# Optimization experiments

Hardware: AMD Instinct MI355X
Metric: run time of the kernel (lower is better)

## Reference

```python
import jax, jax.numpy as jnp
import numpy as np
import math

N = 65536   # number of tree nodes
K = 4       # branching factor of the complete K-ary tree
D = 300     # input_size
H = 256     # hidden_size

def _levels(n, k):
    # complete k-ary tree: level l spans [start, start + k**l)
    levels, start, size = [], 0, 1
    while start < n:
        end = min(start + size, n)
        levels.append((start, end))
        start, size = end, size * k
    return levels

LEVELS = _levels(N, K)

def setup_inputs() -> dict:
    key = jax.random.key(0)
    ks = jax.random.split(key, 16)
    def U(k, shape, s):
        return jax.random.uniform(k, shape, jnp.float32, -s, s)
    s1 = 1.0 / math.sqrt(D + H)
    sfi = 1.0 / math.sqrt(D)
    sfh = 1.0 / math.sqrt(H)
    return {
        "inputs": jax.random.normal(ks[0], (N, D), jnp.float32),
        "ix_w": U(ks[1], (H, D), s1), "ix_b": U(ks[2], (H,), s1),
        "ih_w": U(ks[3], (H, H), s1), "ih_b": U(ks[4], (H,), s1),
        "ux_w": U(ks[5], (H, D), s1), "ux_b": U(ks[6], (H,), s1),
        "uh_w": U(ks[7], (H, H), s1), "uh_b": U(ks[8], (H,), s1),
        "fi_w": U(ks[9], (H, D), sfi), "fi_b": U(ks[10], (H,), sfi),
        "fh_w": U(ks[11], (H, H), sfh), "fh_b": U(ks[12], (H,), sfh),
    }

def reference(inputs, ix_w, ix_b, ih_w, ih_b, ux_w, ux_b, uh_w, uh_b,
              fi_w, fi_b, fh_w, fh_b):
    # Precompute all input projections once (batched over every node).
    ix = inputs @ ix_w.T + ix_b   # [N, H]
    ux = inputs @ ux_w.T + ux_b   # [N, H]
    fi = inputs @ fi_w.T + fi_b   # [N, H]
    h = jnp.zeros((N, H), inputs.dtype)
    c = jnp.zeros((N, H), inputs.dtype)
    # Bottom-up over tree levels (children before parents); level bounds static.
    for (s, e) in reversed(LEVELS):
        node = jnp.arange(s, e)                                   # [L]
        cidx = node[:, None] * K + 1 + jnp.arange(K)[None, :]     # [L, K]
        valid = cidx < N
        cidx = jnp.where(valid, cidx, 0)
        m = valid[..., None].astype(inputs.dtype)                 # [L, K, 1]
        hc = h[cidx] * m                                          # [L, K, H]
        cc = c[cidx] * m
        h_sum = hc.sum(axis=1)                                    # [L, H]
        # per-child forget gate: sigmoid(W_fi x + b_fi + W_fh h_k + b_fh)
        f = jax.nn.sigmoid(fi[s:e][:, None, :]
                           + jnp.einsum('lkh,gh->lkg', hc, fh_w) + fh_b)
        fc = (f * cc).sum(axis=1)                                 # masked via cc
        i = jax.nn.sigmoid(ix[s:e] + h_sum @ ih_w.T + ih_b)
        u = jnp.tanh(ux[s:e] + h_sum @ uh_w.T + uh_b)
        c_new = i * u + fc
        h_new = jnp.tanh(c_new)          # no output gate in this module
        h = h.at[s:e].set(h_new)
        c = c.at[s:e].set(c_new)
    # root node state (matches (next_h, [next_h, next_c]) at the root)
    return h[0], c[0]
```

## Files before the change

kernel.cpp:

```cpp
#include <hip/hip_runtime.h>
#include <hip/hip_bf16.h>


#define NTOT 65536
#define DD   300
#define KP   320
#define HH   256
#define LEAF_START 16384
#define LOG2E 1.4426950408889634f

typedef unsigned short u16;
typedef unsigned int   u32;
typedef __attribute__((ext_vector_type(8))) short bf16x8;
typedef __attribute__((ext_vector_type(4))) float f32x4;

union BF8 { bf16x8 v; u16 u[8]; };

#define OFF_HB    0ull
#define OFF_CB    33554944ull
#define OFF_PRE   67109888ull
#define OFF_WXB   92275712ull
#define OFF_WHB   92767232ull
#define OFF_XB    93160448ull
#define OFF_PIU   135103488ull
#define OFF_PF    146375680ull
#define OFF_BI    168788992ull
#define OFF_BU    168790016ull
#define OFF_BF    168791040ull

__device__ __forceinline__ float frcp(float x) { return __builtin_amdgcn_rcpf(x); }
__device__ __forceinline__ float fex2(float x) { return __builtin_amdgcn_exp2f(x); }
__device__ __forceinline__ float sigm(float x)  { return frcp(1.f + fex2(-LOG2E * x)); }
__device__ __forceinline__ float ftanh(float x) { return 1.f - 2.f * frcp(1.f + fex2(2.f * LOG2E * x)); }

__device__ __forceinline__ u16 f2bf(float f) {
    __hip_bfloat16 b = __float2bfloat16(f);
    u16 u; __builtin_memcpy(&u, &b, 2); return u;
}
__device__ __forceinline__ float bf2f(u16 b) {
    union { u32 u; float f; } v; v.u = ((u32)b) << 16;
    return v.f;
}
__device__ __forceinline__ int lidx(int r, int g) { return (r << 3) | (g ^ (r & 7)); }

__device__ __forceinline__ void gll16(const void* g, void* l) {
    __builtin_amdgcn_global_load_lds(
        (const __attribute__((address_space(1))) unsigned int*)g,
        (__attribute__((address_space(3))) unsigned int*)l, 16, 0, 0);
}

__global__ __launch_bounds__(256) void conv_x(const float* __restrict__ X,
                                              u32* __restrict__ Xb2) {
    const size_t total = (size_t)NTOT * (KP / 2);
    for (size_t id = (size_t)blockIdx.x * 256 + threadIdx.x; id < total;
         id += (size_t)gridDim.x * 256) {
        const int node = (int)(id / (KP / 2));
        const int k    = ((int)(id % (KP / 2))) * 2;
        const float f0 = (k < DD)     ? X[(size_t)node * DD + k]     : 0.f;
        const float f1 = (k + 1 < DD) ? X[(size_t)node * DD + k + 1] : 0.f;
        Xb2[id] = (u32)f2bf(f0) | ((u32)f2bf(f1) << 16);
    }
}

__global__ __launch_bounds__(256) void conv_wx(const float* __restrict__ ixw,
                                               const float* __restrict__ uxw,
                                               const float* __restrict__ fiw,
                                               u32* __restrict__ W2) {
    const int total = 768 * (KP / 2);
    for (int id = blockIdx.x * 256 + threadIdx.x; id < total;
         id += gridDim.x * 256) {
        const int row = id / (KP / 2);
        const int k   = (id % (KP / 2)) * 2;
        const float* src = (row < 256) ? (ixw + (size_t)row * DD)
                         : (row < 512) ? (uxw + (size_t)(row - 256) * DD)
                                       : (fiw + (size_t)(row - 512) * DD);
        const float f0 = (k < DD)     ? src[k]     : 0.f;
        const float f1 = (k + 1 < DD) ? src[k + 1] : 0.f;
        W2[id] = (u32)f2bf(f0) | ((u32)f2bf(f1) << 16);
    }
}

__global__ __launch_bounds__(256) void conv_wh(const float* __restrict__ ihw,
                                               const float* __restrict__ uhw,
                                               const float* __restrict__ fhw,
                                               const float* __restrict__ ixb,
                                               const float* __restrict__ ihb,
                                               const float* __restrict__ uxb,
                                               const float* __restrict__ uhb,
                                               const float* __restrict__ fib,
                                               const float* __restrict__ fhb,
                                               u32* __restrict__ W2,
                                               u16* __restrict__ hb,
                                               u16* __restrict__ cb,
                                               float* __restrict__ bI,
                                               float* __restrict__ bU,
                                               float* __restrict__ bF) {
    if (blockIdx.x == 0) {
        const int t = threadIdx.x;
        hb[(size_t)NTOT * HH + t] = 0;
        cb[(size_t)NTOT * HH + t] = 0;
        bI[t] = ixb[t] + ihb[t];
        bU[t] = uxb[t] + uhb[t];
        bF[t] = fib[t] + fhb[t];
    }
    const int total = 768 * (HH / 2);
    for (int id = blockIdx.x * 256 + threadIdx.x; id < total;
         id += gridDim.x * 256) {
        const int row = id / (HH / 2);
        const int k   = (id % (HH / 2)) * 2;
        const float* src = (row < 256) ? (ihw + (size_t)row * HH)
                         : (row < 512) ? (uhw + (size_t)(row - 256) * HH)
                                       : (fhw + (size_t)(row - 512) * HH);
        W2[id] = (u32)f2bf(src[k]) | ((u32)f2bf(src[k + 1]) << 16);
    }
}

__global__ __launch_bounds__(256) void leaf_gemm(
    const u16* __restrict__ Xb, const u16* __restrict__ Wxb,
    const float* __restrict__ bI, const float* __restrict__ bU,
    u16* __restrict__ hb, u16* __restrict__ cb)
{
    __shared__ bf16x8 Ash[1024];
    __shared__ bf16x8 Bsh[1024];

    const int tid  = threadIdx.x;
    const int lane = tid & 63;
    const int w    = tid >> 6;
    const int wr   = w >> 1, wc = w & 1;
    const int m16  = lane & 15, q = lane >> 4;

    const int row0   = LEAF_START + blockIdx.x * 128;
    const int chbase = blockIdx.y * 64;

    const bf16x8* __restrict__ Xv = (const bf16x8*)Xb;
    const bf16x8* __restrict__ Wv = (const bf16x8*)Wxb;

    f32x4 accI[4][2], accU[4][2];
    #pragma unroll
    for (int mf = 0; mf < 4; ++mf)
        #pragma unroll
        for (int nf = 0; nf < 2; ++nf) { accI[mf][nf] = (f32x4)0.f; accU[mf][nf] = (f32x4)0.f; }

    for (int kt = 0; kt < 5; ++kt) {
        __syncthreads();
        #pragma unroll
        for (int i = 0; i < 4; ++i) {
            const int s = w * 256 + i * 64 + lane;
            const int r = s >> 3, gs = s & 7;
            const int g = gs ^ (r & 7);
            gll16(Xv + (size_t)(row0 + r) * 40 + kt * 8 + g, &Ash[s]);
        }
        #pragma unroll
        for (int i = 0; i < 4; ++i) {
            const int s = w * 256 + i * 64 + lane;
            const int br = s >> 3, gs = s & 7;
            const int g = gs ^ (br & 7);
            const int srow = ((br >> 6) << 8) + chbase + (br & 63);
            gll16(Wv + (size_t)srow * 40 + kt * 8 + g, &Bsh[s]);
        }
        __syncthreads();

        #pragma unroll
        for (int ks = 0; ks < 2; ++ks) {
            const int kg = ks * 4 + q;
            bf16x8 a[4], bIv[2], bUv[2];
            #pragma unroll
            for (int mf = 0; mf < 4; ++mf)
                a[mf] = Ash[lidx(wr * 64 + mf * 16 + m16, kg)];
            #pragma unroll
            for (int nf = 0; nf < 2; ++nf) {
                bIv[nf] = Bsh[lidx(wc * 32 + nf * 16 + m16, kg)];
                bUv[nf] = Bsh[lidx(64 + wc * 32 + nf * 16 + m16, kg)];
            }
            #pragma unroll
            for (int mf = 0; mf < 4; ++mf)
                #pragma unroll
                for (int nf = 0; nf < 2; ++nf) {
                    accI[mf][nf] = __builtin_amdgcn_mfma_f32_16x16x32_bf16(
                        a[mf], bIv[nf], accI[mf][nf], 0, 0, 0);
                    accU[mf][nf] = __builtin_amdgcn_mfma_f32_16x16x32_bf16(
                        a[mf], bUv[nf], accU[mf][nf], 0, 0, 0);
                }
        }
    }

    #pragma unroll
    for (int nf = 0; nf < 2; ++nf) {
        const int ch = chbase + wc * 32 + nf * 16 + m16;
        const float bi = bI[ch];
        const float bu = bU[ch];
        #pragma unroll
        for (int mf = 0; mf < 4; ++mf) {
            #pragma unroll
            for (int r4 = 0; r4 < 4; ++r4) {
                const float cn = sigm(accI[mf][nf][r4] + bi) * ftanh(accU[mf][nf][r4] + bu);
                const int node = row0 + wr * 64 + mf * 16 + q * 4 + r4;
                const size_t off = (size_t)node * HH + ch;
                cb[off] = f2bf(cn);
                hb[off] = f2bf(ftanh(cn));
            }
        }
    }
}

__global__ __launch_bounds__(256) void proj_gemm(const u16* __restrict__ Xb,
                                                 const u16* __restrict__ Wxb,
                                                 u16* __restrict__ pre)
{
    __shared__ bf16x8 Ash[1024];
    __shared__ bf16x8 Bsh[1024];

    const int tid  = threadIdx.x;
    const int lane = tid & 63;
    const int w    = tid >> 6;
    const int wr   = w >> 1, wc = w & 1;
    const int m16  = lane & 15, q = lane >> 4;

    const int row0 = blockIdx.x * 128;
    const int n0   = blockIdx.y * 128;

    const bf16x8* __restrict__ Xv = (const bf16x8*)Xb;
    const bf16x8* __restrict__ Wv = (const bf16x8*)Wxb;

    f32x4 acc[4][4];
    #pragma unroll
    for (int mf = 0; mf < 4; ++mf)
        #pragma unroll
        for (int nf = 0; nf < 4; ++nf) acc[mf][nf] = (f32x4)0.f;

    for (int kt = 0; kt < 5; ++kt) {
        __syncthreads();
        #pragma unroll
        for (int i = 0; i < 4; ++i) {
            const int s = w * 256 + i * 64 + lane;
            const int r = s >> 3, gs = s & 7;
            const int g = gs ^ (r & 7);
            gll16(Xv + (size_t)(row0 + r) * 40 + kt * 8 + g, &Ash[s]);
        }
        #pragma unroll
        for (int i = 0; i < 4; ++i) {
            const int s = w * 256 + i * 64 + lane;
            const int br = s >> 3, gs = s & 7;
            const int g = gs ^ (br & 7);
            gll16(Wv + (size_t)(n0 + br) * 40 + kt * 8 + g, &Bsh[s]);
        }
        __syncthreads();

        #pragma unroll
        for (int ks = 0; ks < 2; ++ks) {
            const int kg = ks * 4 + q;
            bf16x8 a[4], b[4];
            #pragma unroll
            for (int mf = 0; mf < 4; ++mf)
                a[mf] = Ash[lidx(wr * 64 + mf * 16 + m16, kg)];
            #pragma unroll
            for (int nf = 0; nf < 4; ++nf)
                b[nf] = Bsh[lidx(wc * 64 + nf * 16 + m16, kg)];
            #pragma unroll
            for (int mf = 0; mf < 4; ++mf)
                #pragma unroll
                for (int nf = 0; nf < 4; ++nf)
                    acc[mf][nf] = __builtin_amdgcn_mfma_f32_16x16x32_bf16(
                        a[mf], b[nf], acc[mf][nf], 0, 0, 0);
        }
    }

    #pragma unroll
    for (int mf = 0; mf < 4; ++mf)
        #pragma unroll
        for (int nf = 0; nf < 4; ++nf) {
            const int col = n0 + wc * 64 + nf * 16 + m16;
            #pragma unroll
            for (int r4 = 0; r4 < 4; ++r4) {
                const int node = row0 + wr * 64 + mf * 16 + q * 4 + r4;
                pre[(size_t)node * 768 + col] = f2bf(acc[mf][nf][r4]);
            }
        }
}

__global__ __launch_bounds__(256) void rec_gemm(const u16* __restrict__ hb,
                                                const u16* __restrict__ Whb,
                                                u16* __restrict__ projIU,
                                                u16* __restrict__ projF,
                                                int crow0, int L)
{
    __shared__ bf16x8 Ash[1024];
    __shared__ bf16x8 Bsh[1024];

    const int nIUrb = (L + 127) >> 7;
    const int bid   = blockIdx.x;

    bool isIU; int rb, cb_;
    if (bid < nIUrb * 4) { isIU = true;  rb = bid >> 2; cb_ = bid & 3; }
    else { isIU = false; const int b2 = bid - nIUrb * 4; rb = b2 >> 1; cb_ = b2 & 1; }

    const int row0  = rb * 128;
    const int Brow0 = isIU ? cb_ * 128 : 512 + cb_ * 128;
    const int ocol0 = cb_ * 128;
    u16* __restrict__ out = isIU ? projIU : projF;
    const int ostride = isIU ? 512 : 256;

    const int tid  = threadIdx.x;
    const int lane = tid & 63;
    const int w    = tid >> 6;
    const int wr   = w >> 1, wc = w & 1;
    const int m16  = lane & 15, q = lane >> 4;

    const bf16x8* __restrict__ Hv = (const bf16x8*)hb;
    const bf16x8* __restrict__ Wv = (const bf16x8*)Whb;

    f32x4 acc[4][4];
    #pragma unroll
    for (int mf = 0; mf < 4; ++mf)
        #pragma unroll
        for (int nf = 0; nf < 4; ++nf) acc[mf][nf] = (f32x4)0.f;

    for (int kt = 0; kt < 4; ++kt) {
        __syncthreads();
        if (isIU) {
            #pragma unroll
            for (int i = 0; i < 4; ++i) {
                const int G = tid + i * 256;
                const int r = G >> 3, g = G & 7;
                bf16x8 val;
                if (row0 + r < L) {
                    const size_t cg0 = (size_t)(crow0 + 4 * (row0 + r)) * 32 + kt * 8 + g;
                    BF8 x0, x1, x2, x3, o;
                    x0.v = Hv[cg0]; x1.v = Hv[cg0 + 32];
                    x2.v = Hv[cg0 + 64]; x3.v = Hv[cg0 + 96];
                    #pragma unroll
                    for (int j = 0; j < 8; ++j)
                        o.u[j] = f2bf(bf2f(x0.u[j]) + bf2f(x1.u[j])
                                    + bf2f(x2.u[j]) + bf2f(x3.u[j]));
                    val = o.v;
                } else {
                    BF8 z;
                    #pragma unroll
                    for (int j = 0; j < 8; ++j) z.u[j] = 0;
                    val = z.v;
                }
                Ash[lidx(r, g)] = val;
            }
        } else {
            #pragma unroll
            for (int i = 0; i < 4; ++i) {
                const int s = w * 256 + i * 64 + lane;
                const int r = s >> 3, gs = s & 7;
                const int g = gs ^ (r & 7);
                int srow = crow0 + row0 + r;
                if (srow > NTOT) srow = NTOT;
                gll16(Hv + (size_t)srow * 32 + kt * 8 + g, &Ash[s]);
            }
        }
        #pragma unroll
        for (int i = 0; i < 4; ++i) {
            const int s = w * 256 + i * 64 + lane;
            const int br = s >> 3, gs = s & 7;
            const int g = gs ^ (br & 7);
            gll16(Wv + (size_t)(Brow0 + br) * 32 + kt * 8 + g, &Bsh[s]);
        }
        __syncthreads();

        #pragma unroll
        for (int ks = 0; ks < 2; ++ks) {
            const int kg = ks * 4 + q;
            bf16x8 a[4], b[4];
            #pragma unroll
            for (int mf = 0; mf < 4; ++mf)
                a[mf] = Ash[lidx(wr * 64 + mf * 16 + m16, kg)];
            #pragma unroll
            for (int nf = 0; nf < 4; ++nf)
                b[nf] = Bsh[lidx(wc * 64 + nf * 16 + m16, kg)];
            #pragma unroll
            for (int mf = 0; mf < 4; ++mf)
                #pragma unroll
                for (int nf = 0; nf < 4; ++nf)
                    acc[mf][nf] = __builtin_amdgcn_mfma_f32_16x16x32_bf16(
                        a[mf], b[nf], acc[mf][nf], 0, 0, 0);
        }
    }

    #pragma unroll
    for (int mf = 0; mf < 4; ++mf)
        #pragma unroll
        for (int nf = 0; nf < 4; ++nf) {
            const int col = ocol0 + wc * 64 + nf * 16 + m16;
            #pragma unroll
            for (int r4 = 0; r4 < 4; ++r4) {
                const int orow = row0 + wr * 64 + mf * 16 + q * 4 + r4;
                out[(size_t)orow * ostride + col] = f2bf(acc[mf][nf][r4]);
            }
        }
}

__global__ __launch_bounds__(256) void gate_kernel(
    const u32* __restrict__ pre2, const u32* __restrict__ pIU2,
    const u32* __restrict__ pF2,
    const float* __restrict__ bI, const float* __restrict__ bU,
    const float* __restrict__ bF,
    u32* __restrict__ hb2, u32* __restrict__ cb2, float* __restrict__ out,
    int s, int crow0, int L)
{
    const int t    = threadIdx.x;
    const int half = t >> 7;
    const int j2   = t & 127;
    const int nloc = blockIdx.x * 2 + half;
    if (nloc >= L) return;
    const int n = s + nloc;

    const u32 pi = pre2[(size_t)n * 384 + j2];
    const u32 pu = pre2[(size_t)n * 384 + 128 + j2];
    const u32 pf = pre2[(size_t)n * 384 + 256 + j2];
    const u32 ri = pIU2[(size_t)nloc * 256 + j2];
    const u32 ru = pIU2[(size_t)nloc * 256 + 128 + j2];
    const float2 vbi = ((const float2*)bI)[j2];
    const float2 vbu = ((const float2*)bU)[j2];
    const float2 vbf = ((const float2*)bF)[j2];

    const float aI0 = bf2f((u16)pi) + bf2f((u16)ri) + vbi.x;
    const float aI1 = bf2f((u16)(pi >> 16)) + bf2f((u16)(ri >> 16)) + vbi.y;
    const float aU0 = bf2f((u16)pu) + bf2f((u16)ru) + vbu.x;
    const float aU1 = bf2f((u16)(pu >> 16)) + bf2f((u16)(ru >> 16)) + vbu.y;
    const float fp0 = bf2f((u16)pf) + vbf.x;
    const float fp1 = bf2f((u16)(pf >> 16)) + vbf.y;

    float fc0 = 0.f, fc1 = 0.f;
    #pragma unroll
    for (int k = 0; k < 4; ++k) {
        const u32 rf = pF2[(size_t)(4 * nloc + k) * 128 + j2];
        const u32 cc = cb2[(size_t)(crow0 + 4 * nloc + k) * 128 + j2];
        fc0 = fmaf(sigm(fp0 + bf2f((u16)rf)), bf2f((u16)cc), fc0);
        fc1 = fmaf(sigm(fp1 + bf2f((u16)(rf >> 16))), bf2f((u16)(cc >> 16)), fc1);
    }
    const float cn0 = fmaf(sigm(aI0), ftanh(aU0), fc0);
    const float cn1 = fmaf(sigm(aI1), ftanh(aU1), fc1);
    const float hn0 = ftanh(cn0);
    const float hn1 = ftanh(cn1);
    hb2[(size_t)n * 128 + j2] = (u32)f2bf(hn0) | ((u32)f2bf(hn1) << 16);
    cb2[(size_t)n * 128 + j2] = (u32)f2bf(cn0) | ((u32)f2bf(cn1) << 16);
    if (n == 0) {
        ((float2*)out)[j2] = make_float2(hn0, hn1);
        ((float2*)(out + 256))[j2] = make_float2(cn0, cn1);
    }
}

extern "C" void kernel_launch(void* const* d_in, const int* in_sizes, int n_in,
                              void* d_out, int out_size, void* d_ws, size_t ws_size,
                              hipStream_t stream) {
    const float* X   = (const float*)d_in[0];
    const float* ixw = (const float*)d_in[1];
    const float* ixb = (const float*)d_in[2];
    const float* ihw = (const float*)d_in[3];
    const float* ihb = (const float*)d_in[4];
    const float* uxw = (const float*)d_in[5];
    const float* uxb = (const float*)d_in[6];
    const float* uhw = (const float*)d_in[7];
    const float* uhb = (const float*)d_in[8];
    const float* fiw = (const float*)d_in[9];
    const float* fib = (const float*)d_in[10];
    const float* fhw = (const float*)d_in[11];
    const float* fhb = (const float*)d_in[12];
    float* out = (float*)d_out;

    char* ws = (char*)d_ws;
    u16* hb  = (u16*)(ws + OFF_HB);
    u16* cb  = (u16*)(ws + OFF_CB);
    u16* pre = (u16*)(ws + OFF_PRE);
    u16* Wxb = (u16*)(ws + OFF_WXB);
    u16* Whb = (u16*)(ws + OFF_WHB);
    u16* Xb  = (u16*)(ws + OFF_XB);
    u16* pIU = (u16*)(ws + OFF_PIU);
    u16* pF  = (u16*)(ws + OFF_PF);
    float* bI = (float*)(ws + OFF_BI);
    float* bU = (float*)(ws + OFF_BU);
    float* bF = (float*)(ws + OFF_BF);

    conv_wx<<<480, 256, 0, stream>>>(ixw, uxw, fiw, (u32*)Wxb);
    conv_wh<<<384, 256, 0, stream>>>(ihw, uhw, fhw, ixb, ihb, uxb, uhb, fib, fhb,
                                     (u32*)Whb, hb, cb, bI, bU, bF);
    conv_x <<<2048, 256, 0, stream>>>(X, (u32*)Xb);

    leaf_gemm<<<dim3(384, 4), 256, 0, stream>>>(Xb, Wxb, bI, bU, hb, cb);
    proj_gemm<<<dim3(128, 6), 256, 0, stream>>>(Xb, Wxb, pre);

    const int starts[8] = {5461, 1365, 341, 85, 21, 5, 1, 0};
    const int ends[8]   = {16384, 5461, 1365, 341, 85, 21, 5, 1};
    for (int l = 0; l < 8; ++l) {
        const int s = starts[l], e = ends[l];
        const int L = e - s;
        const int crow0 = 4 * s + 1;
        const int nIUrb = (L + 127) >> 7;
        const int nFrb  = (4 * L + 127) >> 7;
        rec_gemm<<<nIUrb * 4 + nFrb * 2, 256, 0, stream>>>(hb, Whb, pIU, pF, crow0, L);
        gate_kernel<<<(L + 1) >> 1, 256, 0, stream>>>(
            (const u32*)pre, (const u32*)pIU, (const u32*)pF, bI, bU, bF,
            (u32*)hb, (u32*)cb, out, s, crow0, L);
    }
}
```

Measured before the change: 213.2 us.

## Fuse conversion kernels, double-buffer GEMM LDS, precompute child h-sums in gate kernel

Merges the three bf16 conversion kernels into a single launch. Leaf, projection and recurrent GEMMs now double-buffer their LDS tiles so the next k-tile's global-to-LDS loads overlap the current MFMAs. Child hidden-state sums are computed ahead of time: a new kernel handles the leaf level, and the gate kernel emits parent sums, so rec_gemm's IU path loads them directly with async LDS loads instead of summing four children per tile. The cost is extra LDS per block, a new workspace buffer, and an extra bf16 rounding of the summed hidden state.

```diff
diff --git a/kernel.cpp b/kernel.cpp
--- a/kernel.cpp
+++ b/kernel.cpp
@@ -13,8 +13,6 @@
 typedef unsigned int   u32;
 typedef __attribute__((ext_vector_type(8))) short bf16x8;
 typedef __attribute__((ext_vector_type(4))) float f32x4;
-
-union BF8 { bf16x8 v; u16 u[8]; };
 
 #define OFF_HB    0ull
 #define OFF_CB    33554944ull
@@ -24,9 +22,10 @@
 #define OFF_XB    93160448ull
 #define OFF_PIU   135103488ull
 #define OFF_PF    146375680ull
-#define OFF_BI    168788992ull
-#define OFF_BU    168790016ull
-#define OFF_BF    168791040ull
+#define OFF_HSB   168788992ull
+#define OFF_BI    177243136ull
+#define OFF_BU    177244160ull
+#define OFF_BF    177245184ull
 
 __device__ __forceinline__ float frcp(float x) { return __builtin_amdgcn_rcpf(x); }
 __device__ __forceinline__ float fex2(float x) { return __builtin_amdgcn_exp2f(x); }
@@ -49,69 +48,61 @@
         (__attribute__((address_space(3))) unsigned int*)l, 16, 0, 0);
 }
 
-__global__ __launch_bounds__(256) void conv_x(const float* __restrict__ X,
-                                              u32* __restrict__ Xb2) {
-    const size_t total = (size_t)NTOT * (KP / 2);
-    for (size_t id = (size_t)blockIdx.x * 256 + threadIdx.x; id < total;
-         id += (size_t)gridDim.x * 256) {
-        const int node = (int)(id / (KP / 2));
-        const int k    = ((int)(id % (KP / 2))) * 2;
-        const float f0 = (k < DD)     ? X[(size_t)node * DD + k]     : 0.f;
-        const float f1 = (k + 1 < DD) ? X[(size_t)node * DD + k + 1] : 0.f;
-        Xb2[id] = (u32)f2bf(f0) | ((u32)f2bf(f1) << 16);
-    }
-}
-
-__global__ __launch_bounds__(256) void conv_wx(const float* __restrict__ ixw,
-                                               const float* __restrict__ uxw,
-                                               const float* __restrict__ fiw,
-                                               u32* __restrict__ W2) {
-    const int total = 768 * (KP / 2);
-    for (int id = blockIdx.x * 256 + threadIdx.x; id < total;
-         id += gridDim.x * 256) {
-        const int row = id / (KP / 2);
-        const int k   = (id % (KP / 2)) * 2;
-        const float* src = (row < 256) ? (ixw + (size_t)row * DD)
-                         : (row < 512) ? (uxw + (size_t)(row - 256) * DD)
-                                       : (fiw + (size_t)(row - 512) * DD);
-        const float f0 = (k < DD)     ? src[k]     : 0.f;
-        const float f1 = (k + 1 < DD) ? src[k + 1] : 0.f;
-        W2[id] = (u32)f2bf(f0) | ((u32)f2bf(f1) << 16);
-    }
-}
-
-__global__ __launch_bounds__(256) void conv_wh(const float* __restrict__ ihw,
-                                               const float* __restrict__ uhw,
-                                               const float* __restrict__ fhw,
-                                               const float* __restrict__ ixb,
-                                               const float* __restrict__ ihb,
-                                               const float* __restrict__ uxb,
-                                               const float* __restrict__ uhb,
-                                               const float* __restrict__ fib,
-                                               const float* __restrict__ fhb,
-                                               u32* __restrict__ W2,
-                                               u16* __restrict__ hb,
-                                               u16* __restrict__ cb,
-                                               float* __restrict__ bI,
-                                               float* __restrict__ bU,
-                                               float* __restrict__ bF) {
-    if (blockIdx.x == 0) {
-        const int t = threadIdx.x;
-        hb[(size_t)NTOT * HH + t] = 0;
-        cb[(size_t)NTOT * HH + t] = 0;
-        bI[t] = ixb[t] + ihb[t];
-        bU[t] = uxb[t] + uhb[t];
-        bF[t] = fib[t] + fhb[t];
-    }
-    const int total = 768 * (HH / 2);
-    for (int id = blockIdx.x * 256 + threadIdx.x; id < total;
-         id += gridDim.x * 256) {
-        const int row = id / (HH / 2);
-        const int k   = (id % (HH / 2)) * 2;
-        const float* src = (row < 256) ? (ihw + (size_t)row * HH)
-                         : (row < 512) ? (uhw + (size_t)(row - 256) * HH)
-                                       : (fhw + (size_t)(row - 512) * HH);
-        W2[id] = (u32)f2bf(src[k]) | ((u32)f2bf(src[k + 1]) << 16);
+__global__ __launch_bounds__(256) void conv_all(
+    const float* __restrict__ X,
+    const float* __restrict__ ixw, const float* __restrict__ uxw,
+    const float* __restrict__ fiw,
+    const float* __restrict__ ihw, const float* __restrict__ uhw,
+    const float* __restrict__ fhw,
+    const float* __restrict__ ixb, const float* __restrict__ ihb,
+    const float* __restrict__ uxb, const float* __restrict__ uhb,
+    const float* __restrict__ fib, const float* __restrict__ fhb,
+    u32* __restrict__ Xb2, u32* __restrict__ Wxb2, u32* __restrict__ Whb2,
+    u16* __restrict__ hb, u16* __restrict__ cb,
+    float* __restrict__ bI, float* __restrict__ bU, float* __restrict__ bF)
+{
+    const int b = blockIdx.x;
+    const int t = threadIdx.x;
+    if (b < 2048) {
+        const size_t total = (size_t)NTOT * 160;
+        for (size_t id = (size_t)b * 256 + t; id < total; id += (size_t)2048 * 256) {
+            const int node = (int)(id / 160);
+            const int k    = ((int)(id % 160)) * 2;
+            const float f0 = (k < DD)     ? X[(size_t)node * DD + k]     : 0.f;
+            const float f1 = (k + 1 < DD) ? X[(size_t)node * DD + k + 1] : 0.f;
+            Xb2[id] = (u32)f2bf(f0) | ((u32)f2bf(f1) << 16);
+        }
+    } else if (b < 2528) {
+        const int b2 = b - 2048;
+        const int total = 768 * 160;
+        for (int id = b2 * 256 + t; id < total; id += 480 * 256) {
+            const int row = id / 160;
+            const int k   = (id % 160) * 2;
+            const float* src = (row < 256) ? (ixw + (size_t)row * DD)
+                             : (row < 512) ? (uxw + (size_t)(row - 256) * DD)
+                                           : (fiw + (size_t)(row - 512) * DD);
+            const float f0 = (k < DD)     ? src[k]     : 0.f;
+            const float f1 = (k + 1 < DD) ? src[k + 1] : 0.f;
+            Wxb2[id] = (u32)f2bf(f0) | ((u32)f2bf(f1) << 16);
+        }
+    } else {
+        const int b3 = b - 2528;
+        if (b3 == 0) {
+            hb[(size_t)NTOT * HH + t] = 0;
+            cb[(size_t)NTOT * HH + t] = 0;
+            bI[t] = ixb[t] + ihb[t];
+            bU[t] = uxb[t] + uhb[t];
+            bF[t] = fib[t] + fhb[t];
+        }
+        const int total = 768 * 128;
+        for (int id = b3 * 256 + t; id < total; id += 384 * 256) {
+            const int row = id / 128;
+            const int k   = (id % 128) * 2;
+            const float* src = (row < 256) ? (ihw + (size_t)row * HH)
+                             : (row < 512) ? (uhw + (size_t)(row - 256) * HH)
+                                           : (fhw + (size_t)(row - 512) * HH);
+            Whb2[id] = (u32)f2bf(src[k]) | ((u32)f2bf(src[k + 1]) << 16);
+        }
     }
 }
 
@@ -120,8 +111,8 @@
     const float* __restrict__ bI, const float* __restrict__ bU,
     u16* __restrict__ hb, u16* __restrict__ cb)
 {
-    __shared__ bf16x8 Ash[1024];
-    __shared__ bf16x8 Bsh[1024];
+    __shared__ bf16x8 Ash[2048];
+    __shared__ bf16x8 Bsh[2048];
 
     const int tid  = threadIdx.x;
     const int lane = tid & 63;
@@ -135,42 +126,48 @@
     const bf16x8* __restrict__ Xv = (const bf16x8*)Xb;
     const bf16x8* __restrict__ Wv = (const bf16x8*)Wxb;
 
-    f32x4 accI[4][2], accU[4][2];
-    #pragma unroll
-    for (int mf = 0; mf < 4; ++mf)
-        #pragma unroll
-        for (int nf = 0; nf < 2; ++nf) { accI[mf][nf] = (f32x4)0.f; accU[mf][nf] = (f32x4)0.f; }
-
-    for (int kt = 0; kt < 5; ++kt) {
-        __syncthreads();
+    auto stage = [&](int kt, int buf) {
+        const int base = buf << 10;
         #pragma unroll
         for (int i = 0; i < 4; ++i) {
-            const int s = w * 256 + i * 64 + lane;
-            const int r = s >> 3, gs = s & 7;
+            const int sI = w * 256 + i * 64 + lane;
+            const int r = sI >> 3, gs = sI & 7;
             const int g = gs ^ (r & 7);
-            gll16(Xv + (size_t)(row0 + r) * 40 + kt * 8 + g, &Ash[s]);
+            gll16(Xv + (size_t)(row0 + r) * 40 + kt * 8 + g, &Ash[base + sI]);
         }
         #pragma unroll
         for (int i = 0; i < 4; ++i) {
-            const int s = w * 256 + i * 64 + lane;
-            const int br = s >> 3, gs = s & 7;
+            const int sI = w * 256 + i * 64 + lane;
+            const int br = sI >> 3, gs = sI & 7;
             const int g = gs ^ (br & 7);
             const int srow = ((br >> 6) << 8) + chbase + (br & 63);
-            gll16(Wv + (size_t)srow * 40 + kt * 8 + g, &Bsh[s]);
-        }
-        __syncthreads();
-
+            gll16(Wv + (size_t)srow * 40 + kt * 8 + g, &Bsh[base + sI]);
+        }
+    };
+
+    f32x4 accI[4][2], accU[4][2];
+    #pragma unroll
+    for (int mf = 0; mf < 4; ++mf)
+        #pragma unroll
+        for (int nf = 0; nf < 2; ++nf) { accI[mf][nf] = (f32x4)0.f; accU[mf][nf] = (f32x4)0.f; }
+
+    stage(0, 0);
+    __syncthreads();
+    for (int kt = 0; kt < 5; ++kt) {
+        const int cur = kt & 1;
+        if (kt < 4) stage(kt + 1, cur ^ 1);
+        const int base = cur << 10;
         #pragma unroll
         for (int ks = 0; ks < 2; ++ks) {
             const int kg = ks * 4 + q;
             bf16x8 a[4], bIv[2], bUv[2];
             #pragma unroll
             for (int mf = 0; mf < 4; ++mf)
-                a[mf] = Ash[lidx(wr * 64 + mf * 16 + m16, kg)];
+                a[mf] = Ash[base + lidx(wr * 64 + mf * 16 + m16, kg)];
             #pragma unroll
             for (int nf = 0; nf < 2; ++nf) {
-                bIv[nf] = Bsh[lidx(wc * 32 + nf * 16 + m16, kg)];
-                bUv[nf] = Bsh[lidx(64 + wc * 32 + nf * 16 + m16, kg)];
+                bIv[nf] = Bsh[base + lidx(wc * 32 + nf * 16 + m16, kg)];
+                bUv[nf] = Bsh[base + lidx(64 + wc * 32 + nf * 16 + m16, kg)];
             }
             #pragma unroll
             for (int mf = 0; mf < 4; ++mf)
@@ -182,6 +179,7 @@
                         a[mf], bUv[nf], accU[mf][nf], 0, 0, 0);
                 }
         }
+        __syncthreads();
     }
 
     #pragma unroll
@@ -207,8 +205,8 @@
                                                  const u16* __restrict__ Wxb,
                                                  u16* __restrict__ pre)
 {
-    __shared__ bf16x8 Ash[1024];
-    __shared__ bf16x8 Bsh[1024];
+    __shared__ bf16x8 Ash[2048];
+    __shared__ bf16x8 Bsh[2048];
 
     const int tid  = threadIdx.x;
     const int lane = tid & 63;
@@ -222,40 +220,46 @@
     const bf16x8* __restrict__ Xv = (const bf16x8*)Xb;
     const bf16x8* __restrict__ Wv = (const bf16x8*)Wxb;
 
+    auto stage = [&](int kt, int buf) {
+        const int base = buf << 10;
+        #pragma unroll
+        for (int i = 0; i < 4; ++i) {
+            const int sI = w * 256 + i * 64 + lane;
+            const int r = sI >> 3, gs = sI & 7;
+            const int g = gs ^ (r & 7);
+            gll16(Xv + (size_t)(row0 + r) * 40 + kt * 8 + g, &Ash[base + sI]);
+        }
+        #pragma unroll
+        for (int i = 0; i < 4; ++i) {
+            const int sI = w * 256 + i * 64 + lane;
+            const int br = sI >> 3, gs = sI & 7;
+            const int g = gs ^ (br & 7);
+            gll16(Wv + (size_t)(n0 + br) * 40 + kt * 8 + g, &Bsh[base + sI]);
+        }
+    };
+
     f32x4 acc[4][4];
     #pragma unroll
     for (int mf = 0; mf < 4; ++mf)
         #pragma unroll
         for (int nf = 0; nf < 4; ++nf) acc[mf][nf] = (f32x4)0.f;
 
+    stage(0, 0);
+    __syncthreads();
     for (int kt = 0; kt < 5; ++kt) {
-        __syncthreads();
-        #pragma unroll
-        for (int i = 0; i < 4; ++i) {
-            const int s = w * 256 + i * 64 + lane;
-            const int r = s >> 3, gs = s & 7;
-            const int g = gs ^ (r & 7);
-            gll16(Xv + (size_t)(row0 + r) * 40 + kt * 8 + g, &Ash[s]);
-        }
-        #pragma unroll
-        for (int i = 0; i < 4; ++i) {
-            const int s = w * 256 + i * 64 + lane;
-            const int br = s >> 3, gs = s & 7;
-            const int g = gs ^ (br & 7);
-            gll16(Wv + (size_t)(n0 + br) * 40 + kt * 8 + g, &Bsh[s]);
-        }
-        __syncthreads();
-
+        const int cur = kt & 1;
+        if (kt < 4) stage(kt + 1, cur ^ 1);
+        const int base = cur << 10;
         #pragma unroll
         for (int ks = 0; ks < 2; ++ks) {
             const int kg = ks * 4 + q;
             bf16x8 a[4], b[4];
             #pragma unroll
             for (int mf = 0; mf < 4; ++mf)
-                a[mf] = Ash[lidx(wr * 64 + mf * 16 + m16, kg)];
+                a[mf] = Ash[base + lidx(wr * 64 + mf * 16 + m16, kg)];
             #pragma unroll
             for (int nf = 0; nf < 4; ++nf)
-                b[nf] = Bsh[lidx(wc * 64 + nf * 16 + m16, kg)];
+                b[nf] = Bsh[base + lidx(wc * 64 + nf * 16 + m16, kg)];
             #pragma unroll
             for (int mf = 0; mf < 4; ++mf)
                 #pragma unroll
@@ -263,6 +267,7 @@
                     acc[mf][nf] = __builtin_amdgcn_mfma_f32_16x16x32_bf16(
                         a[mf], b[nf], acc[mf][nf], 0, 0, 0);
         }
+        __syncthreads();
     }
 
     #pragma unroll
@@ -278,25 +283,45 @@
         }
 }
 
+__global__ __launch_bounds__(256) void hsum_big(const u32* __restrict__ hb2,
+                                                u32* __restrict__ hsumb2)
+{
+    const int id = blockIdx.x * 256 + threadIdx.x;
+    const int total = 12288 * 128;
+    if (id >= total) return;
+    const int ploc = id >> 7, j2 = id & 127;
+    const int p = 4096 + ploc;
+    const int c0 = 4 * p + 1;
+    float s0 = 0.f, s1 = 0.f;
+    #pragma unroll
+    for (int k = 0; k < 4; ++k) {
+        const u32 v = hb2[(size_t)(c0 + k) * 128 + j2];
+        s0 += bf2f((u16)v);
+        s1 += bf2f((u16)(v >> 16));
+    }
+    hsumb2[(size_t)p * 128 + j2] = (u32)f2bf(s0) | ((u32)f2bf(s1) << 16);
+}
+
 __global__ __launch_bounds__(256) void rec_gemm(const u16* __restrict__ hb,
+                                                const u16* __restrict__ hsumb,
                                                 const u16* __restrict__ Whb,
                                                 u16* __restrict__ projIU,
                                                 u16* __restrict__ projF,
-                                                int crow0, int L)
+                                                int crow0, int prow0, int L)
 {
-    __shared__ bf16x8 Ash[1024];
-    __shared__ bf16x8 Bsh[1024];
+    __shared__ bf16x8 Ash[2048];
+    __shared__ bf16x8 Bsh[2048];
 
     const int nIUrb = (L + 127) >> 7;
     const int bid   = blockIdx.x;
 
-    bool isIU; int rb, cb_;
-    if (bid < nIUrb * 4) { isIU = true;  rb = bid >> 2; cb_ = bid & 3; }
-    else { isIU = false; const int b2 = bid - nIUrb * 4; rb = b2 >> 1; cb_ = b2 & 1; }
+    bool isIU; int rb, cbk;
+    if (bid < nIUrb * 4) { isIU = true;  rb = bid >> 2; cbk = bid & 3; }
+    else { isIU = false; const int b2 = bid - nIUrb * 4; rb = b2 >> 1; cbk = b2 & 1; }
 
     const int row0  = rb * 128;
-    const int Brow0 = isIU ? cb_ * 128 : 512 + cb_ * 128;
-    const int ocol0 = cb_ * 128;
+    const int Brow0 = isIU ? cbk * 128 : 512 + cbk * 128;
+    const int ocol0 = cbk * 128;
     u16* __restrict__ out = isIU ? projIU : projF;
     const int ostride = isIU ? 512 : 256;
 
@@ -306,71 +331,52 @@
     const int wr   = w >> 1, wc = w & 1;
     const int m16  = lane & 15, q = lane >> 4;
 
-    const bf16x8* __restrict__ Hv = (const bf16x8*)hb;
+    const bf16x8* __restrict__ Av = isIU ? (const bf16x8*)hsumb : (const bf16x8*)hb;
     const bf16x8* __restrict__ Wv = (const bf16x8*)Whb;
 
+    auto stage = [&](int kt, int buf) {
+        const int base = buf << 10;
+        #pragma unroll
+        for (int i = 0; i < 4; ++i) {
+            const int sI = w * 256 + i * 64 + lane;
+            const int r = sI >> 3, gs = sI & 7;
+            const int g = gs ^ (r & 7);
+            int arow;
+            if (isIU) arow = prow0 + row0 + r;
+            else { arow = crow0 + row0 + r; if (arow > NTOT) arow = NTOT; }
+            gll16(Av + (size_t)arow * 32 + kt * 8 + g, &Ash[base + sI]);
+        }
+        #pragma unroll
+        for (int i = 0; i < 4; ++i) {
+            const int sI = w * 256 + i * 64 + lane;
+            const int br = sI >> 3, gs = sI & 7;
+            const int g = gs ^ (br & 7);
+            gll16(Wv + (size_t)(Brow0 + br) * 32 + kt * 8 + g, &Bsh[base + sI]);
+        }
+    };
+
     f32x4 acc[4][4];
     #pragma unroll
     for (int mf = 0; mf < 4; ++mf)
         #pragma unroll
         for (int nf = 0; nf < 4; ++nf) acc[mf][nf] = (f32x4)0.f;
 
+    stage(0, 0);
+    __syncthreads();
     for (int kt = 0; kt < 4; ++kt) {
-        __syncthreads();
-        if (isIU) {
-            #pragma unroll
-            for (int i = 0; i < 4; ++i) {
-                const int G = tid + i * 256;
-                const int r = G >> 3, g = G & 7;
-                bf16x8 val;
-                if (row0 + r < L) {
-                    const size_t cg0 = (size_t)(crow0 + 4 * (row0 + r)) * 32 + kt * 8 + g;
-                    BF8 x0, x1, x2, x3, o;
-                    x0.v = Hv[cg0]; x1.v = Hv[cg0 + 32];
-                    x2.v = Hv[cg0 + 64]; x3.v = Hv[cg0 + 96];
-                    #pragma unroll
-                    for (int j = 0; j < 8; ++j)
-                        o.u[j] = f2bf(bf2f(x0.u[j]) + bf2f(x1.u[j])
-                                    + bf2f(x2.u[j]) + bf2f(x3.u[j]));
-                    val = o.v;
-                } else {
-                    BF8 z;
-                    #pragma unroll
-                    for (int j = 0; j < 8; ++j) z.u[j] = 0;
-                    val = z.v;
-                }
-                Ash[lidx(r, g)] = val;
-            }
-        } else {
-            #pragma unroll
-            for (int i = 0; i < 4; ++i) {
-                const int s = w * 256 + i * 64 + lane;
-                const int r = s >> 3, gs = s & 7;
-                const int g = gs ^ (r & 7);
-                int srow = crow0 + row0 + r;
-                if (srow > NTOT) srow = NTOT;
-                gll16(Hv + (size_t)srow * 32 + kt * 8 + g, &Ash[s]);
-            }
-        }
-        #pragma unroll
-        for (int i = 0; i < 4; ++i) {
-            const int s = w * 256 + i * 64 + lane;
-            const int br = s >> 3, gs = s & 7;
-            const int g = gs ^ (br & 7);
-            gll16(Wv + (size_t)(Brow0 + br) * 32 + kt * 8 + g, &Bsh[s]);
-        }
-        __syncthreads();
-
+        const int cur = kt & 1;
+        if (kt < 3) stage(kt + 1, cur ^ 1);
+        const int base = cur << 10;
         #pragma unroll
         for (int ks = 0; ks < 2; ++ks) {
             const int kg = ks * 4 + q;
             bf16x8 a[4], b[4];
             #pragma unroll
             for (int mf = 0; mf < 4; ++mf)
-                a[mf] = Ash[lidx(wr * 64 + mf * 16 + m16, kg)];
+                a[mf] = Ash[base + lidx(wr * 64 + mf * 16 + m16, kg)];
             #pragma unroll
             for (int nf = 0; nf < 4; ++nf)
-                b[nf] = Bsh[lidx(wc * 64 + nf * 16 + m16, kg)];
+                b[nf] = Bsh[base + lidx(wc * 64 + nf * 16 + m16, kg)];
             #pragma unroll
             for (int mf = 0; mf < 4; ++mf)
                 #pragma unroll
@@ -378,6 +384,7 @@
                     acc[mf][nf] = __builtin_amdgcn_mfma_f32_16x16x32_bf16(
                         a[mf], b[nf], acc[mf][nf], 0, 0, 0);
         }
+        __syncthreads();
     }
 
     #pragma unroll
@@ -398,50 +405,91 @@
     const u32* __restrict__ pF2,
     const float* __restrict__ bI, const float* __restrict__ bU,
     const float* __restrict__ bF,
-    u32* __restrict__ hb2, u32* __restrict__ cb2, float* __restrict__ out,
-    int s, int crow0, int L)
+    u32* __restrict__ hb2, u32* __restrict__ cb2, u32* __restrict__ hsumb2,
+    float* __restrict__ out, int s, int crow0, int L)
 {
-    const int t    = threadIdx.x;
-    const int half = t >> 7;
-    const int j2   = t & 127;
-    const int nloc = blockIdx.x * 2 + half;
-    if (nloc >= L) return;
-    const int n = s + nloc;
-
-    const u32 pi = pre2[(size_t)n * 384 + j2];
-    const u32 pu = pre2[(size_t)n * 384 + 128 + j2];
-    const u32 pf = pre2[(size_t)n * 384 + 256 + j2];
-    const u32 ri = pIU2[(size_t)nloc * 256 + j2];
-    const u32 ru = pIU2[(size_t)nloc * 256 + 128 + j2];
+    const int t  = threadIdx.x;
+    const int j2 = t & 127;
     const float2 vbi = ((const float2*)bI)[j2];
     const float2 vbu = ((const float2*)bU)[j2];
     const float2 vbf = ((const float2*)bF)[j2];
 
-    const float aI0 = bf2f((u16)pi) + bf2f((u16)ri) + vbi.x;
-    const float aI1 = bf2f((u16)(pi >> 16)) + bf2f((u16)(ri >> 16)) + vbi.y;
-    const float aU0 = bf2f((u16)pu) + bf2f((u16)ru) + vbu.x;
-    const float aU1 = bf2f((u16)(pu >> 16)) + bf2f((u16)(ru >> 16)) + vbu.y;
-    const float fp0 = bf2f((u16)pf) + vbf.x;
-    const float fp1 = bf2f((u16)(pf >> 16)) + vbf.y;
-
-    float fc0 = 0.f, fc1 = 0.f;
-    #pragma unroll
-    for (int k = 0; k < 4; ++k) {
-        const u32 rf = pF2[(size_t)(4 * nloc + k) * 128 + j2];
-        const u32 cc = cb2[(size_t)(crow0 + 4 * nloc + k) * 128 + j2];
-        fc0 = fmaf(sigm(fp0 + bf2f((u16)rf)), bf2f((u16)cc), fc0);
-        fc1 = fmaf(sigm(fp1 + bf2f((u16)(rf >> 16))), bf2f((u16)(cc >> 16)), fc1);
-    }
-    const float cn0 = fmaf(sigm(aI0), ftanh(aU0), fc0);
-    const float cn1 = fmaf(sigm(aI1), ftanh(aU1), fc1);
-    const float hn0 = ftanh(cn0);
-    const float hn1 = ftanh(cn1);
-    hb2[(size_t)n * 128 + j2] = (u32)f2bf(hn0) | ((u32)f2bf(hn1) << 16);
-    cb2[(size_t)n * 128 + j2] = (u32)f2bf(cn0) | ((u32)f2bf(cn1) << 16);
-    if (n == 0) {
+    if (L == 1) {
+        if (t >= 128) return;
+        const u32 pi = pre2[j2];
+        const u32 pu = pre2[128 + j2];
+        const u32 pf = pre2[256 + j2];
+        const u32 ri = pIU2[j2];
+        const u32 ru = pIU2[128 + j2];
+        const float aI0 = bf2f((u16)pi) + bf2f((u16)ri) + vbi.x;
+        const float aI1 = bf2f((u16)(pi >> 16)) + bf2f((u16)(ri >> 16)) + vbi.y;
+        const float aU0 = bf2f((u16)pu) + bf2f((u16)ru) + vbu.x;
+        const float aU1 = bf2f((u16)(pu >> 16)) + bf2f((u16)(ru >> 16)) + vbu.y;
+        const float fp0 = bf2f((u16)pf) + vbf.x;
+        const float fp1 = bf2f((u16)(pf >> 16)) + vbf.y;
+        float fc0 = 0.f, fc1 = 0.f;
+        #pragma unroll
+        for (int kk = 0; kk < 4; ++kk) {
+            const u32 rf = pF2[(size_t)kk * 128 + j2];
+            const u32 cc = cb2[(size_t)(crow0 + kk) * 128 + j2];
+            fc0 = fmaf(sigm(fp0 + bf2f((u16)rf)), bf2f((u16)cc), fc0);
+            fc1 = fmaf(sigm(fp1 + bf2f((u16)(rf >> 16))), bf2f((u16)(cc >> 16)), fc1);
+        }
+        const float cn0 = fmaf(sigm(aI0), ftanh(aU0), fc0);
+        const float cn1 = fmaf(sigm(aI1), ftanh(aU1), fc1);
+        const float hn0 = ftanh(cn0);
+        const float hn1 = ftanh(cn1);
+        hb2[j2] = (u32)f2bf(hn0) | ((u32)f2bf(hn1) << 16);
+        cb2[j2] = (u32)f2bf(cn0) | ((u32)f2bf(cn1) << 16);
         ((float2*)out)[j2] = make_float2(hn0, hn1);
         ((float2*)(out + 256))[j2] = make_float2(cn0, cn1);
-    }
+        return;
+    }
+
+    const int ng = (L + 3) >> 2;
+    const int g  = blockIdx.x * 2 + (t >> 7);
+    if (g >= ng) return;
+    const int p = ((s - 1) >> 2) + g;
+
+    float hs0 = 0.f, hs1 = 0.f;
+    #pragma unroll
+    for (int k = 0; k < 4; ++k) {
+        const int nloc = 4 * g + k;
+        const int n = s + nloc;
+        if (nloc < L) {
+            const u32 pi = pre2[(size_t)n * 384 + j2];
+            const u32 pu = pre2[(size_t)n * 384 + 128 + j2];
+            const u32 pf = pre2[(size_t)n * 384 + 256 + j2];
+            const u32 ri = pIU2[(size_t)nloc * 256 + j2];
+            const u32 ru = pIU2[(size_t)nloc * 256 + 128 + j2];
+            const float aI0 = bf2f((u16)pi) + bf2f((u16)ri) + vbi.x;
+            const float aI1 = bf2f((u16)(pi >> 16)) + bf2f((u16)(ri >> 16)) + vbi.y;
+            const float aU0 = bf2f((u16)pu) + bf2f((u16)ru) + vbu.x;
+            const float aU1 = bf2f((u16)(pu >> 16)) + bf2f((u16)(ru >> 16)) + vbu.y;
+            const float fp0 = bf2f((u16)pf) + vbf.x;
+            const float fp1 = bf2f((u16)(pf >> 16)) + vbf.y;
+            float fc0 = 0.f, fc1 = 0.f;
+            #pragma unroll
+            for (int kk = 0; kk < 4; ++kk) {
+                const u32 rf = pF2[(size_t)(4 * nloc + kk) * 128 + j2];
+                const u32 cc = cb2[(size_t)(crow0 + 4 * nloc + kk) * 128 + j2];
+                fc0 = fmaf(sigm(fp0 + bf2f((u16)rf)), bf2f((u16)cc), fc0);
+                fc1 = fmaf(sigm(fp1 + bf2f((u16)(rf >> 16))), bf2f((u16)(cc >> 16)), fc1);
+            }
+            const float cn0 = fmaf(sigm(aI0), ftanh(aU0), fc0);
+            const float cn1 = fmaf(sigm(aI1), ftanh(aU1), fc1);
+            const float hn0 = ftanh(cn0);
+            const float hn1 = ftanh(cn1);
+            hb2[(size_t)n * 128 + j2] = (u32)f2bf(hn0) | ((u32)f2bf(hn1) << 16);
+            cb2[(size_t)n * 128 + j2] = (u32)f2bf(cn0) | ((u32)f2bf(cn1) << 16);
+            hs0 += hn0; hs1 += hn1;
+        } else {
+            const u32 v = hb2[(size_t)n * 128 + j2];
+            hs0 += bf2f((u16)v);
+            hs1 += bf2f((u16)(v >> 16));
+        }
+    }
+    hsumb2[(size_t)p * 128 + j2] = (u32)f2bf(hs0) | ((u32)f2bf(hs1) << 16);
 }
 
 extern "C" void kernel_launch(void* const* d_in, const int* in_sizes, int n_in,
@@ -463,25 +511,26 @@
     float* out = (float*)d_out;
 
     char* ws = (char*)d_ws;
-    u16* hb  = (u16*)(ws + OFF_HB);
-    u16* cb  = (u16*)(ws + OFF_CB);
-    u16* pre = (u16*)(ws + OFF_PRE);
-    u16* Wxb = (u16*)(ws + OFF_WXB);
-    u16* Whb = (u16*)(ws + OFF_WHB);
-    u16* Xb  = (u16*)(ws + OFF_XB);
-    u16* pIU = (u16*)(ws + OFF_PIU);
-    u16* pF  = (u16*)(ws + OFF_PF);
+    u16* hb   = (u16*)(ws + OFF_HB);
+    u16* cb   = (u16*)(ws + OFF_CB);
+    u16* pre  = (u16*)(ws + OFF_PRE);
+    u16* Wxb  = (u16*)(ws + OFF_WXB);
+    u16* Whb  = (u16*)(ws + OFF_WHB);
+    u16* Xb   = (u16*)(ws + OFF_XB);
+    u16* pIU  = (u16*)(ws + OFF_PIU);
+    u16* pF   = (u16*)(ws + OFF_PF);
+    u16* hsb  = (u16*)(ws + OFF_HSB);
     float* bI = (float*)(ws + OFF_BI);
     float* bU = (float*)(ws + OFF_BU);
     float* bF = (float*)(ws + OFF_BF);
 
-    conv_wx<<<480, 256, 0, stream>>>(ixw, uxw, fiw, (u32*)Wxb);
-    conv_wh<<<384, 256, 0, stream>>>(ihw, uhw, fhw, ixb, ihb, uxb, uhb, fib, fhb,
-                                     (u32*)Whb, hb, cb, bI, bU, bF);
-    conv_x <<<2048, 256, 0, stream>>>(X, (u32*)Xb);
+    conv_all<<<2912, 256, 0, stream>>>(X, ixw, uxw, fiw, ihw, uhw, fhw,
+        ixb, ihb, uxb, uhb, fib, fhb,
+        (u32*)Xb, (u32*)Wxb, (u32*)Whb, hb, cb, bI, bU, bF);
 
     leaf_gemm<<<dim3(384, 4), 256, 0, stream>>>(Xb, Wxb, bI, bU, hb, cb);
     proj_gemm<<<dim3(128, 6), 256, 0, stream>>>(Xb, Wxb, pre);
+    hsum_big<<<6144, 256, 0, stream>>>((const u32*)hb, (u32*)hsb);
 
     const int starts[8] = {5461, 1365, 341, 85, 21, 5, 1, 0};
     const int ends[8]   = {16384, 5461, 1365, 341, 85, 21, 5, 1};
@@ -491,9 +540,11 @@
         const int crow0 = 4 * s + 1;
         const int nIUrb = (L + 127) >> 7;
         const int nFrb  = (4 * L + 127) >> 7;
-        rec_gemm<<<nIUrb * 4 + nFrb * 2, 256, 0, stream>>>(hb, Whb, pIU, pF, crow0, L);
-        gate_kernel<<<(L + 1) >> 1, 256, 0, stream>>>(
+        rec_gemm<<<nIUrb * 4 + nFrb * 2, 256, 0, stream>>>(hb, hsb, Whb, pIU, pF,
+                                                           crow0, s, L);
+        const int ng = (L + 3) >> 2;
+        gate_kernel<<<(ng + 1) >> 1, 256, 0, stream>>>(
             (const u32*)pre, (const u32*)pIU, (const u32*)pF, bI, bU, bF,
-            (u32*)hb, (u32*)cb, out, s, crow0, L);
-    }
-}
+            (u32*)hb, (u32*)cb, (u32*)hsb, out, s, crow0, L);
+    }
+}
```

New measurement: 198.8 us. -6.7%, faster.
